# Kernel tuning notes

Hardware: AMD Instinct MI355X
Metric: run time of the kernel (lower is better)

The kernel has to match this reference:

```python
import jax, jax.numpy as jnp
import numpy as np

B, S, H, F, E, K = 8, 4096, 256, 512, 16, 2
EPS = 1e-5


def setup_inputs() -> dict:
    key = jax.random.key(0)
    ks = jax.random.split(key, 9)
    sc = 0.02
    return {
        "x": jax.random.normal(ks[0], (B, S, H), dtype=jnp.float32),
        "gate_w": jax.random.normal(ks[1], (H, E), dtype=jnp.float32) * sc,
        "gate_b": jnp.zeros((E,), dtype=jnp.float32),
        "w1": jax.random.normal(ks[2], (E, H, F), dtype=jnp.float32) * sc,
        "b1": jnp.zeros((E, F), dtype=jnp.float32),
        "w2": jax.random.normal(ks[3], (E, F, H), dtype=jnp.float32) * sc,
        "b2": jnp.zeros((E, H), dtype=jnp.float32),
        "gamma": jnp.ones((H,), dtype=jnp.float32),
        "beta": jnp.zeros((H,), dtype=jnp.float32),
    }


def reference(x, gate_w, gate_b, w1, b1, w2, b2, gamma, beta):
    # gating: top-k over expert logits, softmax over the k selected logits
    gate_logits = x @ gate_w + gate_b                      # [B,S,E]
    topk_vals, topk_idx = jax.lax.top_k(gate_logits, K)    # [B,S,K]
    topk_w = jax.nn.softmax(topk_vals, axis=-1)            # [B,S,K]

    # naive dense MoE: every expert runs over every token (matches source)
    h = jax.nn.relu(jnp.einsum('bsh,ehf->bsef', x, w1) + b1)   # [B,S,E,F]
    expert_out = jnp.einsum('bsef,efh->bseh', h, w2) + b2       # [B,S,E,H]

    # select top-k expert outputs and combine with gate weights
    sel = jnp.take_along_axis(expert_out, topk_idx[:, :, :, None], axis=2)  # [B,S,K,H]
    moe = jnp.sum(topk_w[..., None] * sel, axis=2)              # [B,S,H]

    # residual + LayerNorm
    y = x + moe
    mu = jnp.mean(y, axis=-1, keepdims=True)
    var = jnp.var(y, axis=-1, keepdims=True)
    return (y - mu) / jnp.sqrt(var + EPS) * gamma + beta
```

## Files before the change

kernel.cpp:

```cpp
#include <hip/hip_runtime.h>
#include <hip/hip_bf16.h>

typedef __bf16 bf16_t;
typedef __bf16 bf16x8 __attribute__((ext_vector_type(8)));
typedef __bf16 bf16x4 __attribute__((ext_vector_type(4)));
typedef float f32x4 __attribute__((ext_vector_type(4)));

#define NB 8
#define NS 4096
#define NH 256
#define NF 512
#define NE 16
#define NTOK (NB*NS)
#define TT 64
#define NCH 16

#define XS_U(r,u) (((r) << 5) + ((u) ^ ((r) & 7)))
#define HS_U(r,u) (((r) << 2) + ((u) ^ (((r) >> 2) & 3)))

__global__ __launch_bounds__(256) void transpose_kernel(
    const float* __restrict__ w1, const float* __restrict__ w2,
    bf16_t* __restrict__ w1t, bf16_t* __restrict__ w2t)
{
    __shared__ float tile[32][33];
    int bid = blockIdx.x;
    const float* src; bf16_t* dst; int R, C; int isw1;
    if (bid < 2048) { src = w1; dst = w1t; R = NH; C = NF; isw1 = 1; }
    else            { bid -= 2048; src = w2; dst = w2t; R = NF; C = NH; isw1 = 0; }
    int e = bid >> 7;
    int t = bid & 127;
    int tcols = C / 32;
    int tr = (t / tcols) * 32, tc = (t % tcols) * 32;
    src += (size_t)e * R * C;
    dst += (size_t)e * R * C;
    int tx = threadIdx.x & 31, ty0 = threadIdx.x >> 5;
    #pragma unroll
    for (int i = 0; i < 4; i++) {
        int ty = ty0 + i * 8;
        tile[ty][tx] = src[(size_t)(tr + ty) * C + tc + tx];
    }
    __syncthreads();
    if (threadIdx.x < 128) {
        int j = threadIdx.x & 31;
        int g = threadIdx.x >> 5;
        bf16x8 v;
        #pragma unroll
        for (int jj = 0; jj < 8; jj++)
            v[jj] = (bf16_t)tile[g * 8 + jj][j];
        size_t idx;
        if (isw1) {
            int f  = tc + j;
            int kb = tr + g * 8;
            idx = (size_t)f * NH + ((((kb >> 3) ^ (f & 7))) << 3);
        } else {
            int h  = tc + j;
            int fb = tr + g * 8;
            idx = ((size_t)(fb >> 5) * NH + h) * 32 + (fb & 31);
        }
        *(bf16x8*)(dst + idx) = v;
    }
}

__global__ __launch_bounds__(256) void gate_kernel(
    const float* __restrict__ x, const float* __restrict__ gate_w,
    const float* __restrict__ gate_b,
    int* __restrict__ counts, int* __restrict__ bucket_enc,
    float* __restrict__ bucket_gw, bf16_t* __restrict__ xb)
{
    __shared__ float gws[NH][NE];
    __shared__ int lcnt[NE];
    __shared__ int gbase[NE];

    for (int i = threadIdx.x; i < NH * NE; i += 256)
        gws[i >> 4][i & 15] = gate_w[i];
    if (threadIdx.x < NE) lcnt[threadIdx.x] = 0;
    __syncthreads();

    int tok = blockIdx.x * 256 + threadIdx.x;
    const float4* xr = (const float4*)(x + (size_t)tok * NH);
    bf16x4* xbr = (bf16x4*)(xb + (size_t)tok * NH);
    float acc[NE];
    #pragma unroll
    for (int e = 0; e < NE; e++) acc[e] = gate_b[e];
    for (int h4 = 0; h4 < NH / 4; h4++) {
        float4 xv = xr[h4];
        bf16x4 xo;
        xo[0] = (bf16_t)xv.x; xo[1] = (bf16_t)xv.y;
        xo[2] = (bf16_t)xv.z; xo[3] = (bf16_t)xv.w;
        xbr[h4] = xo;
        #pragma unroll
        for (int j = 0; j < 4; j++) {
            float xs = (j == 0) ? xv.x : (j == 1) ? xv.y : (j == 2) ? xv.z : xv.w;
            int h = h4 * 4 + j;
            #pragma unroll
            for (int e = 0; e < NE; e++) acc[e] += xs * gws[h][e];
        }
    }
    float v0 = -1e30f, v1 = -1e30f; int i0 = 0, i1 = 0;
    #pragma unroll
    for (int e = 0; e < NE; e++) {
        float a = acc[e];
        if (a > v0)      { v1 = v0; i1 = i0; v0 = a; i0 = e; }
        else if (a > v1) { v1 = a; i1 = e; }
    }
    float e1 = __expf(v1 - v0);
    float s  = 1.f + e1;
    int   pe[2] = { i0, i1 };
    float pg[2] = { 1.f / s, e1 / s };
    int   po[2];
    po[0] = atomicAdd(&lcnt[i0], 1);
    po[1] = atomicAdd(&lcnt[i1], 1);
    __syncthreads();
    if (threadIdx.x < NE)
        gbase[threadIdx.x] = atomicAdd(&counts[threadIdx.x], lcnt[threadIdx.x]);
    __syncthreads();
    #pragma unroll
    for (int k = 0; k < 2; k++) {
        int e = pe[k];
        int pos = gbase[e] + po[k];
        bucket_enc[e * NTOK + pos] = tok | (k << 20);
        bucket_gw [e * NTOK + pos] = pg[k];
    }
}

__global__ __launch_bounds__(256, 2) void moe_kernel(
    const bf16_t* __restrict__ xb,
    const bf16_t* __restrict__ w1t,
    const float*  __restrict__ b1,
    const bf16_t* __restrict__ w2t,
    const float*  __restrict__ b2,
    const int* __restrict__ counts,
    const int* __restrict__ bucket_enc,
    const float* __restrict__ bucket_gw,
    bf16_t* __restrict__ pairbuf)
{
    __shared__ uint4 Xs4[TT * 32];
    __shared__ uint4 W1s4[2][1024];
    __shared__ uint4 Hs4[2][TT * 4];
    __shared__ int   tok_s[TT];
    __shared__ float gw_s[TT];

    int flat = blockIdx.x;
    int e     = (flat & 7) * 2 + ((flat >> 3) & 1);
    int tile0 = flat >> 4;
    int n_e = counts[e];
    int wave = threadIdx.x >> 6;
    int lane = threadIdx.x & 63;
    int l15 = lane & 15, q = lane >> 4;

    const bf16_t* w1te = w1t + (size_t)e * NF * NH;
    const bf16_t* w2te = w2t + (size_t)e * NF * NH;

    int ntiles = (n_e + TT - 1) / TT;
    for (int tile = tile0; tile < ntiles; tile += 64) {
        int tstart = tile * TT;
        __syncthreads();
        if (threadIdx.x < TT) {
            int slot = tstart + threadIdx.x;
            if (slot < n_e) {
                tok_s[threadIdx.x] = bucket_enc[e * NTOK + slot];
                gw_s [threadIdx.x] = bucket_gw [e * NTOK + slot];
            } else { tok_s[threadIdx.x] = 0; gw_s[threadIdx.x] = 0.f; }
        }
        __syncthreads();
        {
            int c  = threadIdx.x & 31;
            int r0 = threadIdx.x >> 5;
            #pragma unroll
            for (int i = 0; i < 8; i++) {
                int r = r0 + i * 8;
                int tok = tok_s[r] & 0xFFFFF;
                Xs4[XS_U(r, c)] = ((const uint4*)(xb + (size_t)tok * NH))[c];
            }
            const uint4* gw1 = (const uint4*)w1te;
            #pragma unroll
            for (int i = 0; i < 4; i++)
                W1s4[0][i * 256 + threadIdx.x] = gw1[i * 256 + threadIdx.x];
        }
        __syncthreads();

        f32x4 oacc[4][4];
        #pragma unroll
        for (int a = 0; a < 4; a++)
            #pragma unroll
            for (int b = 0; b < 4; b++) { f32x4 z = {0.f,0.f,0.f,0.f}; oacc[a][b] = z; }

        for (int ch = 0; ch < NCH; ch++) {
            int buf = ch & 1;
            uint4 pf[4];
            bool do_pf = (ch + 1 < NCH);
            if (do_pf) {
                const uint4* gw1 = (const uint4*)w1te + (size_t)(ch + 1) * 1024;
                #pragma unroll
                for (int i = 0; i < 4; i++) pf[i] = gw1[i * 256 + threadIdx.x];
            }
            bf16x8 bf2[4];
            #pragma unroll
            for (int nt = 0; nt < 4; nt++) {
                int hh = wave * 64 + nt * 16 + l15;
                bf2[nt] = *(const bf16x8*)&w2te[(((size_t)ch * NH + hh) << 5) + q * 8];
            }
            f32x4 hacc[2]; { f32x4 z = {0.f,0.f,0.f,0.f}; hacc[0] = z; hacc[1] = z; }
            const bf16_t* w1s = (const bf16_t*)W1s4[buf];
            __builtin_amdgcn_s_setprio(1);
            #pragma unroll
            for (int ks = 0; ks < 8; ks++) {
                bf16x8 afrag = *(const bf16x8*)&Xs4[XS_U(wave * 16 + l15, ks * 4 + q)];
                #pragma unroll
                for (int n = 0; n < 2; n++) {
                    int fl = n * 16 + l15;
                    bf16x8 bfrag = *(const bf16x8*)&w1s[fl * NH + ((((ks * 4 + q) ^ (fl & 7))) << 3)];
                    hacc[n] = __builtin_amdgcn_mfma_f32_16x16x32_bf16(afrag, bfrag, hacc[n], 0, 0, 0);
                }
            }
            __builtin_amdgcn_s_setprio(0);
            {
                bf16_t* hsb = (bf16_t*)Hs4[buf];
                #pragma unroll
                for (int n = 0; n < 2; n++) {
                    int f = ch * 32 + n * 16 + l15;
                    float bv = b1[e * NF + f];
                    #pragma unroll
                    for (int r = 0; r < 4; r++) {
                        float v = hacc[n][r] + bv;
                        v = v > 0.f ? v : 0.f;
                        int row = wave * 16 + q * 4 + r;
                        hsb[row * 32 + ((n * 16 + l15) ^ (((row >> 2) & 3) << 3))] = (bf16_t)v;
                    }
                }
            }
            if (do_pf) {
                #pragma unroll
                for (int i = 0; i < 4; i++)
                    W1s4[buf ^ 1][i * 256 + threadIdx.x] = pf[i];
            }
            __syncthreads();
            __builtin_amdgcn_s_setprio(1);
            #pragma unroll
            for (int mt = 0; mt < 4; mt++) {
                bf16x8 afrag = *(const bf16x8*)&Hs4[buf][HS_U(mt * 16 + l15, q)];
                #pragma unroll
                for (int nt = 0; nt < 4; nt++) {
                    oacc[mt][nt] = __builtin_amdgcn_mfma_f32_16x16x32_bf16(afrag, bf2[nt], oacc[mt][nt], 0, 0, 0);
                }
            }
            __builtin_amdgcn_s_setprio(0);
        }
        {
            bf16_t* xsb = (bf16_t*)Xs4;
            #pragma unroll
            for (int nt = 0; nt < 4; nt++) {
                int col = wave * 64 + nt * 16 + l15;
                float b2v = b2[e * NH + col];
                #pragma unroll
                for (int mt = 0; mt < 4; mt++) {
                    #pragma unroll
                    for (int r = 0; r < 4; r++) {
                        int row = mt * 16 + q * 4 + r;
                        float v = (oacc[mt][nt][r] + b2v) * gw_s[row];
                        xsb[row * NH + (col ^ ((row & 7) << 3))] = (bf16_t)v;
                    }
                }
            }
        }
        __syncthreads();
        {
            int nrows = n_e - tstart; if (nrows > TT) nrows = TT;
            int c  = threadIdx.x & 31;
            int r0 = threadIdx.x >> 5;
            #pragma unroll
            for (int i = 0; i < 8; i++) {
                int r = r0 + i * 8;
                if (r < nrows) {
                    int enc = tok_s[r];
                    int tok = enc & 0xFFFFF;
                    int k   = enc >> 20;
                    ((uint4*)(pairbuf + ((size_t)(tok * 2 + k)) * NH))[c] = Xs4[XS_U(r, c)];
                }
            }
        }
    }
}

__global__ __launch_bounds__(256) void ln_kernel(
    const float* __restrict__ x, const bf16_t* __restrict__ pairbuf,
    const float* __restrict__ gamma, const float* __restrict__ beta,
    float* __restrict__ out)
{
    int tok  = blockIdx.x * 4 + (threadIdx.x >> 6);
    int lane = threadIdx.x & 63;
    float4 xv = *(const float4*)(x + (size_t)tok * NH + lane * 4);
    bf16x4 p0 = *(const bf16x4*)(pairbuf + (size_t)(tok * 2)     * NH + lane * 4);
    bf16x4 p1 = *(const bf16x4*)(pairbuf + (size_t)(tok * 2 + 1) * NH + lane * 4);
    float y0 = xv.x + (float)p0[0] + (float)p1[0];
    float y1 = xv.y + (float)p0[1] + (float)p1[1];
    float y2 = xv.z + (float)p0[2] + (float)p1[2];
    float y3 = xv.w + (float)p0[3] + (float)p1[3];
    float s  = y0 + y1 + y2 + y3;
    float s2 = y0 * y0 + y1 * y1 + y2 * y2 + y3 * y3;
    #pragma unroll
    for (int o = 32; o > 0; o >>= 1) {
        s  += __shfl_xor(s, o);
        s2 += __shfl_xor(s2, o);
    }
    float mu   = s * (1.f / NH);
    float var  = s2 * (1.f / NH) - mu * mu;
    float rstd = rsqrtf(var + 1e-5f);
    float4 gv = *(const float4*)(gamma + lane * 4);
    float4 bv = *(const float4*)(beta  + lane * 4);
    float4 o4;
    o4.x = (y0 - mu) * rstd * gv.x + bv.x;
    o4.y = (y1 - mu) * rstd * gv.y + bv.y;
    o4.z = (y2 - mu) * rstd * gv.z + bv.z;
    o4.w = (y3 - mu) * rstd * gv.w + bv.w;
    *(float4*)(out + (size_t)tok * NH + lane * 4) = o4;
}

extern "C" void kernel_launch(void* const* d_in, const int* in_sizes, int n_in,
                              void* d_out, int out_size, void* d_ws, size_t ws_size,
                              hipStream_t stream) {
    const float* x      = (const float*)d_in[0];
    const float* gate_w = (const float*)d_in[1];
    const float* gate_b = (const float*)d_in[2];
    const float* w1     = (const float*)d_in[3];
    const float* b1     = (const float*)d_in[4];
    const float* w2     = (const float*)d_in[5];
    const float* b2     = (const float*)d_in[6];
    const float* gamma  = (const float*)d_in[7];
    const float* beta   = (const float*)d_in[8];
    float* out = (float*)d_out;

    char* ws = (char*)d_ws;
    const size_t MB = 1024 * 1024;
    int*    counts     = (int*)ws;
    int*    bucket_enc = (int*)(ws + 256);
    float*  bucket_gw  = (float*)(ws + 256 + 2 * MB);
    bf16_t* w1t        = (bf16_t*)(ws + 256 + 4 * MB);
    bf16_t* w2t        = (bf16_t*)(ws + 256 + 8 * MB);
    bf16_t* xb         = (bf16_t*)(ws + 256 + 12 * MB);
    bf16_t* pairbuf    = (bf16_t*)(ws + 256 + 28 * MB);

    hipMemsetAsync(counts, 0, 256, stream);
    transpose_kernel<<<4096, 256, 0, stream>>>(w1, w2, w1t, w2t);
    gate_kernel<<<128, 256, 0, stream>>>(x, gate_w, gate_b, counts, bucket_enc, bucket_gw, xb);
    moe_kernel<<<1024, 256, 0, stream>>>(xb, w1t, b1, w2t, b2, counts, bucket_enc, bucket_gw, pairbuf);
    ln_kernel<<<NTOK / 4, 256, 0, stream>>>(x, pairbuf, gamma, beta, out);
}
```

Baseline: 266.1 us.

## Keep X tile in registers, async-load W1 to LDS, write outputs directly

The MoE kernel no longer stages the gathered token tile in LDS. Each lane keeps its X fragments in registers, and the MFMA operand order is swapped so results come out transposed. The W1 chunk prefetch now uses global_load_lds direct-to-LDS loads instead of a register round-trip. The epilogue writes bf16x4 results straight to pairbuf without staging in LDS and without the extra barrier. Freeing the shared memory allows occupancy 3 with 768 blocks, in exchange for higher register pressure and less-coalesced 8-byte scattered stores.

```diff
diff --git a/kernel.cpp b/kernel.cpp
--- a/kernel.cpp
+++ b/kernel.cpp
@@ -14,9 +14,13 @@
 #define NTOK (NB*NS)
 #define TT 64
 #define NCH 16
-
-#define XS_U(r,u) (((r) << 5) + ((u) ^ ((r) & 7)))
-#define HS_U(r,u) (((r) << 2) + ((u) ^ (((r) >> 2) & 3)))
+#define HS_STRIDE 40
+
+__device__ __forceinline__ void load_lds16(const void* g, void* l) {
+    __builtin_amdgcn_global_load_lds(
+        (const __attribute__((address_space(1))) unsigned int*)g,
+        (__attribute__((address_space(3))) unsigned int*)l, 16, 0, 0);
+}
 
 __global__ __launch_bounds__(256) void transpose_kernel(
     const float* __restrict__ w1, const float* __restrict__ w2,
@@ -123,7 +127,7 @@
     }
 }
 
-__global__ __launch_bounds__(256, 2) void moe_kernel(
+__global__ __launch_bounds__(256, 3) void moe_kernel(
     const bf16_t* __restrict__ xb,
     const bf16_t* __restrict__ w1t,
     const float*  __restrict__ b1,
@@ -134,15 +138,16 @@
     const float* __restrict__ bucket_gw,
     bf16_t* __restrict__ pairbuf)
 {
-    __shared__ uint4 Xs4[TT * 32];
     __shared__ uint4 W1s4[2][1024];
-    __shared__ uint4 Hs4[2][TT * 4];
+    __shared__ __align__(16) bf16_t Hs[2][TT][HS_STRIDE];
     __shared__ int   tok_s[TT];
     __shared__ float gw_s[TT];
 
     int flat = blockIdx.x;
-    int e     = (flat & 7) * 2 + ((flat >> 3) & 1);
-    int tile0 = flat >> 4;
+    int xcd  = flat & 7;
+    int j    = flat >> 3;
+    int e    = xcd * 2 + (j & 1);
+    int tile0 = j >> 1;
     int n_e = counts[e];
     int wave = threadIdx.x >> 6;
     int lane = threadIdx.x & 63;
@@ -152,7 +157,7 @@
     const bf16_t* w2te = w2t + (size_t)e * NF * NH;
 
     int ntiles = (n_e + TT - 1) / TT;
-    for (int tile = tile0; tile < ntiles; tile += 64) {
+    for (int tile = tile0; tile < ntiles; tile += 48) {
         int tstart = tile * TT;
         __syncthreads();
         if (threadIdx.x < TT) {
@@ -163,20 +168,18 @@
             } else { tok_s[threadIdx.x] = 0; gw_s[threadIdx.x] = 0.f; }
         }
         __syncthreads();
+
         {
-            int c  = threadIdx.x & 31;
-            int r0 = threadIdx.x >> 5;
-            #pragma unroll
-            for (int i = 0; i < 8; i++) {
-                int r = r0 + i * 8;
-                int tok = tok_s[r] & 0xFFFFF;
-                Xs4[XS_U(r, c)] = ((const uint4*)(xb + (size_t)tok * NH))[c];
-            }
             const uint4* gw1 = (const uint4*)w1te;
             #pragma unroll
             for (int i = 0; i < 4; i++)
-                W1s4[0][i * 256 + threadIdx.x] = gw1[i * 256 + threadIdx.x];
-        }
+                load_lds16(gw1 + i * 256 + threadIdx.x, &W1s4[0][i * 256 + threadIdx.x]);
+        }
+        int mytok = tok_s[wave * 16 + l15] & 0xFFFFF;
+        const uint4* xrow = (const uint4*)(xb + (size_t)mytok * NH);
+        uint4 xf[8];
+        #pragma unroll
+        for (int ks = 0; ks < 8; ks++) xf[ks] = xrow[ks * 4 + q];
         __syncthreads();
 
         f32x4 oacc[4][4];
@@ -187,12 +190,12 @@
 
         for (int ch = 0; ch < NCH; ch++) {
             int buf = ch & 1;
-            uint4 pf[4];
-            bool do_pf = (ch + 1 < NCH);
-            if (do_pf) {
+            if (ch + 1 < NCH) {
                 const uint4* gw1 = (const uint4*)w1te + (size_t)(ch + 1) * 1024;
                 #pragma unroll
-                for (int i = 0; i < 4; i++) pf[i] = gw1[i * 256 + threadIdx.x];
+                for (int i = 0; i < 4; i++)
+                    load_lds16(gw1 + i * 256 + threadIdx.x,
+                               &W1s4[buf ^ 1][i * 256 + threadIdx.x]);
             }
             bf16x8 bf2[4];
             #pragma unroll
@@ -202,81 +205,61 @@
             }
             f32x4 hacc[2]; { f32x4 z = {0.f,0.f,0.f,0.f}; hacc[0] = z; hacc[1] = z; }
             const bf16_t* w1s = (const bf16_t*)W1s4[buf];
-            __builtin_amdgcn_s_setprio(1);
             #pragma unroll
             for (int ks = 0; ks < 8; ks++) {
-                bf16x8 afrag = *(const bf16x8*)&Xs4[XS_U(wave * 16 + l15, ks * 4 + q)];
+                bf16x8 xfrag = *(const bf16x8*)&xf[ks];
                 #pragma unroll
                 for (int n = 0; n < 2; n++) {
                     int fl = n * 16 + l15;
-                    bf16x8 bfrag = *(const bf16x8*)&w1s[fl * NH + ((((ks * 4 + q) ^ (fl & 7))) << 3)];
-                    hacc[n] = __builtin_amdgcn_mfma_f32_16x16x32_bf16(afrag, bfrag, hacc[n], 0, 0, 0);
+                    bf16x8 wf = *(const bf16x8*)&w1s[fl * NH + ((((ks * 4 + q) ^ (fl & 7))) << 3)];
+                    hacc[n] = __builtin_amdgcn_mfma_f32_16x16x32_bf16(wf, xfrag, hacc[n], 0, 0, 0);
                 }
             }
-            __builtin_amdgcn_s_setprio(0);
-            {
-                bf16_t* hsb = (bf16_t*)Hs4[buf];
-                #pragma unroll
-                for (int n = 0; n < 2; n++) {
-                    int f = ch * 32 + n * 16 + l15;
-                    float bv = b1[e * NF + f];
-                    #pragma unroll
-                    for (int r = 0; r < 4; r++) {
-                        float v = hacc[n][r] + bv;
-                        v = v > 0.f ? v : 0.f;
-                        int row = wave * 16 + q * 4 + r;
-                        hsb[row * 32 + ((n * 16 + l15) ^ (((row >> 2) & 3) << 3))] = (bf16_t)v;
-                    }
+            #pragma unroll
+            for (int n = 0; n < 2; n++) {
+                int f0 = ch * 32 + n * 16 + q * 4;
+                float4 b1v = *(const float4*)&b1[e * NF + f0];
+                bf16x4 hv;
+                #pragma unroll
+                for (int r = 0; r < 4; r++) {
+                    float v = hacc[n][r] + ((const float*)&b1v)[r];
+                    v = v > 0.f ? v : 0.f;
+                    hv[r] = (bf16_t)v;
                 }
-            }
-            if (do_pf) {
-                #pragma unroll
-                for (int i = 0; i < 4; i++)
-                    W1s4[buf ^ 1][i * 256 + threadIdx.x] = pf[i];
+                *(bf16x4*)&Hs[buf][wave * 16 + l15][n * 16 + q * 4] = hv;
             }
             __syncthreads();
-            __builtin_amdgcn_s_setprio(1);
             #pragma unroll
             for (int mt = 0; mt < 4; mt++) {
-                bf16x8 afrag = *(const bf16x8*)&Hs4[buf][HS_U(mt * 16 + l15, q)];
+                bf16x8 hf = *(const bf16x8*)&Hs[buf][mt * 16 + l15][q * 8];
                 #pragma unroll
                 for (int nt = 0; nt < 4; nt++) {
-                    oacc[mt][nt] = __builtin_amdgcn_mfma_f32_16x16x32_bf16(afrag, bf2[nt], oacc[mt][nt], 0, 0, 0);
+                    oacc[mt][nt] = __builtin_amdgcn_mfma_f32_16x16x32_bf16(bf2[nt], hf, oacc[mt][nt], 0, 0, 0);
                 }
             }
-            __builtin_amdgcn_s_setprio(0);
-        }
-        {
-            bf16_t* xsb = (bf16_t*)Xs4;
+        }
+        int nrows = n_e - tstart; if (nrows > TT) nrows = TT;
+        float4 b2v[4];
+        #pragma unroll
+        for (int nt = 0; nt < 4; nt++)
+            b2v[nt] = *(const float4*)&b2[e * NH + wave * 64 + nt * 16 + q * 4];
+        #pragma unroll
+        for (int mt = 0; mt < 4; mt++) {
+            int trow = mt * 16 + l15;
+            int enc  = tok_s[trow];
+            float gw = gw_s[trow];
+            bool valid = trow < nrows;
+            int tok = enc & 0xFFFFF;
+            int kk  = enc >> 20;
+            bf16_t* orow = pairbuf + ((size_t)(tok * 2 + kk)) * NH;
             #pragma unroll
             for (int nt = 0; nt < 4; nt++) {
-                int col = wave * 64 + nt * 16 + l15;
-                float b2v = b2[e * NH + col];
-                #pragma unroll
-                for (int mt = 0; mt < 4; mt++) {
-                    #pragma unroll
-                    for (int r = 0; r < 4; r++) {
-                        int row = mt * 16 + q * 4 + r;
-                        float v = (oacc[mt][nt][r] + b2v) * gw_s[row];
-                        xsb[row * NH + (col ^ ((row & 7) << 3))] = (bf16_t)v;
-                    }
-                }
-            }
-        }
-        __syncthreads();
-        {
-            int nrows = n_e - tstart; if (nrows > TT) nrows = TT;
-            int c  = threadIdx.x & 31;
-            int r0 = threadIdx.x >> 5;
-            #pragma unroll
-            for (int i = 0; i < 8; i++) {
-                int r = r0 + i * 8;
-                if (r < nrows) {
-                    int enc = tok_s[r];
-                    int tok = enc & 0xFFFFF;
-                    int k   = enc >> 20;
-                    ((uint4*)(pairbuf + ((size_t)(tok * 2 + k)) * NH))[c] = Xs4[XS_U(r, c)];
-                }
+                int col = wave * 64 + nt * 16 + q * 4;
+                bf16x4 ov;
+                #pragma unroll
+                for (int r = 0; r < 4; r++)
+                    ov[r] = (bf16_t)((oacc[mt][nt][r] + ((const float*)&b2v[nt])[r]) * gw);
+                if (valid) *(bf16x4*)&orow[col] = ov;
             }
         }
     }
@@ -343,6 +326,6 @@
     hipMemsetAsync(counts, 0, 256, stream);
     transpose_kernel<<<4096, 256, 0, stream>>>(w1, w2, w1t, w2t);
     gate_kernel<<<128, 256, 0, stream>>>(x, gate_w, gate_b, counts, bucket_enc, bucket_gw, xb);
-    moe_kernel<<<1024, 256, 0, stream>>>(xb, w1t, b1, w2t, b2, counts, bucket_enc, bucket_gw, pairbuf);
+    moe_kernel<<<768, 256, 0, stream>>>(xb, w1t, b1, w2t, b2, counts, bucket_enc, bucket_gw, pairbuf);
     ln_kernel<<<NTOK / 4, 256, 0, stream>>>(x, pairbuf, gamma, beta, out);
 }
```

Result: faster. 249.0 us (-6.4%).
